# Optimization experiments

Measured on AMD Instinct MI355X. Metric: run time of the kernel, lower is better.

Reference implementation:

```python
import jax, jax.numpy as jnp
import numpy as np

B, C, H, W = 32, 192, 56, 56
DILATIONS = (1, 3, 5)
EPS = 1e-5


def setup_inputs() -> dict:
    key = jax.random.key(0)
    ks = jax.random.split(key, 4)
    x = jax.random.normal(ks[0], (B, C, H, W), dtype=jnp.float32)
    # learned params (per original torch init where it matters for math)
    bias = jnp.zeros((1, C, 1, 1), dtype=jnp.float32)            # LearnableBias
    conv_w = jax.random.normal(ks[1], (3, C, 1, 3, 3), dtype=jnp.float32) * 0.1  # depthwise kernels (OIHW, I=1)
    conv_b = jax.random.normal(ks[2], (3, C), dtype=jnp.float32) * 0.01
    move1 = jnp.zeros((3, C), dtype=jnp.float32)
    alpha = jnp.full((3, C), 0.25, dtype=jnp.float32)            # PReLU default init
    move2 = jnp.zeros((3, C), dtype=jnp.float32)
    ln_gamma = jnp.ones((C,), dtype=jnp.float32)
    ln_beta = jnp.zeros((C,), dtype=jnp.float32)
    return {"x": x, "bias": bias, "conv_w": conv_w, "conv_b": conv_b,
            "move1": move1, "alpha": alpha, "move2": move2,
            "ln_gamma": ln_gamma, "ln_beta": ln_beta}


def _per_ch(v):
    # (C,) -> (1,C,1,1) broadcastable over NCHW
    return v[None, :, None, None]


def reference(x, bias, conv_w, conv_b, move1, alpha, move2, ln_gamma, ln_beta):
    c = x.shape[1]
    xb = x + bias  # LearnableBias
    out = jnp.zeros_like(x)
    for i, d in enumerate(DILATIONS):
        # depthwise 3x3 dilated conv, 'same' padding => pad = d for k=3
        y = jax.lax.conv_general_dilated(
            xb, conv_w[i],
            window_strides=(1, 1),
            padding=((d, d), (d, d)),
            rhs_dilation=(d, d),
            feature_group_count=c,
            dimension_numbers=("NCHW", "OIHW", "NCHW"),
        ) + _per_ch(conv_b[i])
        # RPReLU: shift, per-channel PReLU, shift
        y = y - _per_ch(move1[i])
        y = jnp.where(y >= 0, y, _per_ch(alpha[i]) * y)
        y = y + _per_ch(move2[i])
        out = out + y
    # LayerNorm over channel dim (torch applies it on NHWC last axis == channels)
    mean = out.mean(axis=1, keepdims=True)
    var = out.var(axis=1, keepdims=True)  # biased, matches torch LayerNorm
    out = (out - mean) * jax.lax.rsqrt(var + EPS)
    out = out * _per_ch(ln_gamma) + _per_ch(ln_beta)
    return out
```

## Files before the change

kernel.cpp:

```cpp
#include <hip/hip_runtime.h>

#define C 192
#define H 56
#define W 56
#define HW (H * W)
#define CHW (C * HW)
#define NB 32
#define PPS 36
#define EPSLN 1e-5f

#define CTL_SHL1 0x101
#define CTL_SHL2 0x102
#define CTL_SHR1 0x111
#define CTL_SHR2 0x112

template<int CTRL>
__device__ __forceinline__ float dppf(float v) {
    return __int_as_float(__builtin_amdgcn_update_dpp(
        0, __float_as_int(v), CTRL, 0xf, 0xf, true));
}

struct __attribute__((aligned(16))) f4 { float x, y, z, w; };

__device__ __forceinline__ f4 f4z() { return {0.f, 0.f, 0.f, 0.f}; }
__device__ __forceinline__ f4 f4b(float s) { return {s, s, s, s}; }
__device__ __forceinline__ f4 fma4(f4 a, float s, f4 c) {
    return { fmaf(a.x, s, c.x), fmaf(a.y, s, c.y),
             fmaf(a.z, s, c.z), fmaf(a.w, s, c.w) };
}
__device__ __forceinline__ f4 shp1(f4 v){ return { v.y, v.z, v.w, dppf<CTL_SHL1>(v.x) }; }
__device__ __forceinline__ f4 shm1(f4 v){ return { dppf<CTL_SHR1>(v.w), v.x, v.y, v.z }; }
__device__ __forceinline__ f4 shp3(f4 v){ return { v.w, dppf<CTL_SHL1>(v.x),
                                                   dppf<CTL_SHL1>(v.y), dppf<CTL_SHL1>(v.z) }; }
__device__ __forceinline__ f4 shm3(f4 v){ return { dppf<CTL_SHR1>(v.y), dppf<CTL_SHR1>(v.z),
                                                   dppf<CTL_SHR1>(v.w), v.x }; }
__device__ __forceinline__ f4 shp5(f4 v){ return { dppf<CTL_SHL1>(v.y), dppf<CTL_SHL1>(v.z),
                                                   dppf<CTL_SHL1>(v.w), dppf<CTL_SHL2>(v.x) }; }
__device__ __forceinline__ f4 shm5(f4 v){ return { dppf<CTL_SHR2>(v.w), dppf<CTL_SHR1>(v.x),
                                                   dppf<CTL_SHR1>(v.y), dppf<CTL_SHR1>(v.z) }; }

__device__ __forceinline__ f4 prelu_acc(f4 acc, f4 y, float a) {
    acc.x += fmaxf(y.x, 0.f) + a * fminf(y.x, 0.f);
    acc.y += fmaxf(y.y, 0.f) + a * fminf(y.y, 0.f);
    acc.z += fmaxf(y.z, 0.f) + a * fminf(y.z, 0.f);
    acc.w += fmaxf(y.w, 0.f) + a * fminf(y.w, 0.f);
    return acc;
}

__global__ void prep_kernel(const float* __restrict__ bias,
                            const float* __restrict__ conv_w,
                            const float* __restrict__ conv_b,
                            const float* __restrict__ move1,
                            const float* __restrict__ alpha,
                            const float* __restrict__ move2,
                            const float* __restrict__ ln_g,
                            const float* __restrict__ ln_b,
                            float* __restrict__ pp, float* __restrict__ gb) {
    const int c = threadIdx.x;
    if (c >= C) return;
    float* pc = pp + c * PPS;
    #pragma unroll
    for (int i = 0; i < 3; ++i)
        #pragma unroll
        for (int k = 0; k < 9; ++k)
            pc[i * 9 + k] = conv_w[(size_t)(i * C + c) * 9 + k];
    #pragma unroll
    for (int i = 0; i < 3; ++i) {
        pc[27 + i] = conv_b[i * C + c] - move1[i * C + c];
        pc[30 + i] = alpha[i * C + c];
    }
    pc[33] = bias[c];
    pc[34] = move2[0 * C + c] + move2[1 * C + c] + move2[2 * C + c];
    pc[35] = 0.f;
    gb[2 * c]     = ln_g[c];
    gb[2 * c + 1] = ln_b[c];
}

__global__ __launch_bounds__(256, 3) void msgdc_kernel(
    const float* __restrict__ x, const float* __restrict__ pp,
    const float* __restrict__ gb, float* __restrict__ out)
{
    __shared__ float tile[C * W];
    __shared__ float sred[4][16][8];

    const int t = threadIdx.x;
    const int lane = t & 63;
    const int wv = __builtin_amdgcn_readfirstlane(t >> 6);
    const int l = lane & 15;
    const bool act = (l < 14);
    const float act_f = act ? 1.f : 0.f;
    const int lw = act ? 4 * l : 52;

    const int blk = blockIdx.x;
    const int gid = (blk & 7) * 224 + (blk >> 3);
    const int b = gid / H;
    const int h = gid - b * H;

    const bool vr[7] = { h >= 5, h >= 3, h >= 1, true,
                         h <= H - 2, h <= H - 4, h <= H - 6 };
    const int  ro[7] = { -5 * W, -3 * W, -1 * W, 0, 1 * W, 3 * W, 5 * W };
    float vm[7];
    #pragma unroll
    for (int k = 0; k < 7; ++k) vm[k] = vr[k] ? 1.f : 0.f;

    const int cbase = wv * 48 + (lane >> 4);
    const float* xc = x + (size_t)b * CHW + (size_t)cbase * HW + h * W + lw;

    f4 cur[7], nxt[7];
    #pragma unroll
    for (int k = 0; k < 7; ++k)
        nxt[k] = vr[k] ? *(const f4*)(xc + ro[k]) : f4z();

    f4 s4 = f4z(), q4 = f4z();

    #pragma unroll 2
    for (int j = 0; j < 12; ++j) {
        const int c = cbase + 4 * j;
        #pragma unroll
        for (int k = 0; k < 7; ++k) cur[k] = nxt[k];

        const float* pc = pp + c * PPS;
        float wf[36];
        #pragma unroll
        for (int k = 0; k < 9; ++k)
            *(f4*)(wf + 4 * k) = *(const f4*)(pc + 4 * k);

        if (j < 11) {
            const float* xn = xc + (size_t)(4 * (j + 1)) * HW;
            #pragma unroll
            for (int k = 0; k < 7; ++k)
                nxt[k] = vr[k] ? *(const f4*)(xn + ro[k]) : f4z();
        }

        const float bs = wf[33];
        f4 r[7];
        #pragma unroll
        for (int k = 0; k < 7; ++k) {
            const float bk = bs * vm[k] * act_f;
            r[k].x = fmaf(cur[k].x, act_f, bk);
            r[k].y = fmaf(cur[k].y, act_f, bk);
            r[k].z = fmaf(cur[k].z, act_f, bk);
            r[k].w = fmaf(cur[k].w, act_f, bk);
        }

        f4 acc = f4b(wf[34]);
        {
            f4 y = f4b(wf[27]);
            y = fma4(shm1(r[2]), wf[0], y);
            y = fma4(r[2],       wf[1], y);
            y = fma4(shp1(r[2]), wf[2], y);
            y = fma4(shm1(r[3]), wf[3], y);
            y = fma4(r[3],       wf[4], y);
            y = fma4(shp1(r[3]), wf[5], y);
            y = fma4(shm1(r[4]), wf[6], y);
            y = fma4(r[4],       wf[7], y);
            y = fma4(shp1(r[4]), wf[8], y);
            acc = prelu_acc(acc, y, wf[30]);
        }
        {
            f4 y = f4b(wf[28]);
            y = fma4(shm3(r[1]), wf[9],  y);
            y = fma4(r[1],       wf[10], y);
            y = fma4(shp3(r[1]), wf[11], y);
            y = fma4(shm3(r[3]), wf[12], y);
            y = fma4(r[3],       wf[13], y);
            y = fma4(shp3(r[3]), wf[14], y);
            y = fma4(shm3(r[5]), wf[15], y);
            y = fma4(r[5],       wf[16], y);
            y = fma4(shp3(r[5]), wf[17], y);
            acc = prelu_acc(acc, y, wf[31]);
        }
        {
            f4 y = f4b(wf[29]);
            y = fma4(shm5(r[0]), wf[18], y);
            y = fma4(r[0],       wf[19], y);
            y = fma4(shp5(r[0]), wf[20], y);
            y = fma4(shm5(r[3]), wf[21], y);
            y = fma4(r[3],       wf[22], y);
            y = fma4(shp5(r[3]), wf[23], y);
            y = fma4(shm5(r[6]), wf[24], y);
            y = fma4(r[6],       wf[25], y);
            y = fma4(shp5(r[6]), wf[26], y);
            acc = prelu_acc(acc, y, wf[32]);
        }

        s4.x += acc.x; s4.y += acc.y; s4.z += acc.z; s4.w += acc.w;
        q4.x = fmaf(acc.x, acc.x, q4.x); q4.y = fmaf(acc.y, acc.y, q4.y);
        q4.z = fmaf(acc.z, acc.z, q4.z); q4.w = fmaf(acc.w, acc.w, q4.w);

        if (act) *(f4*)(tile + c * W + lw) = acc;
    }

    #pragma unroll
    for (int m = 16; m <= 32; m <<= 1) {
        s4.x += __shfl_xor(s4.x, m, 64); s4.y += __shfl_xor(s4.y, m, 64);
        s4.z += __shfl_xor(s4.z, m, 64); s4.w += __shfl_xor(s4.w, m, 64);
        q4.x += __shfl_xor(q4.x, m, 64); q4.y += __shfl_xor(q4.y, m, 64);
        q4.z += __shfl_xor(q4.z, m, 64); q4.w += __shfl_xor(q4.w, m, 64);
    }
    if (lane < 14) {
        *(f4*)&sred[wv][lane][0] = s4;
        *(f4*)&sred[wv][lane][4] = q4;
    }
    __syncthreads();

    f4 S = f4z(), Q = f4z();
    #pragma unroll
    for (int w2 = 0; w2 < 4; ++w2) {
        const f4 a = *(const f4*)&sred[w2][l][0];
        const f4 bq = *(const f4*)&sred[w2][l][4];
        S.x += a.x; S.y += a.y; S.z += a.z; S.w += a.w;
        Q.x += bq.x; Q.y += bq.y; Q.z += bq.z; Q.w += bq.w;
    }
    const float inv = 1.f / (float)C;
    f4 mean = { S.x * inv, S.y * inv, S.z * inv, S.w * inv };
    f4 rstd = { rsqrtf(Q.x * inv - mean.x * mean.x + EPSLN),
                rsqrtf(Q.y * inv - mean.y * mean.y + EPSLN),
                rsqrtf(Q.z * inv - mean.z * mean.z + EPSLN),
                rsqrtf(Q.w * inv - mean.w * mean.w + EPSLN) };

    float* ob = out + (size_t)b * CHW + (size_t)cbase * HW + h * W + lw;
    #pragma unroll 2
    for (int j = 0; j < 12; ++j) {
        const int c = cbase + 4 * j;
        const float ga = gb[2 * c], be = gb[2 * c + 1];
        if (act) {
            const f4 v = *(const f4*)(tile + c * W + lw);
            f4 o;
            o.x = fmaf((v.x - mean.x) * rstd.x, ga, be);
            o.y = fmaf((v.y - mean.y) * rstd.y, ga, be);
            o.z = fmaf((v.z - mean.z) * rstd.z, ga, be);
            o.w = fmaf((v.w - mean.w) * rstd.w, ga, be);
            *(f4*)(ob + (size_t)(4 * j) * HW) = o;
        }
    }
}

extern "C" void kernel_launch(void* const* d_in, const int* in_sizes, int n_in,
                              void* d_out, int out_size, void* d_ws, size_t ws_size,
                              hipStream_t stream) {
    const float* x       = (const float*)d_in[0];
    const float* bias    = (const float*)d_in[1];
    const float* conv_w  = (const float*)d_in[2];
    const float* conv_b  = (const float*)d_in[3];
    const float* move1   = (const float*)d_in[4];
    const float* alpha   = (const float*)d_in[5];
    const float* move2   = (const float*)d_in[6];
    const float* ln_g    = (const float*)d_in[7];
    const float* ln_b    = (const float*)d_in[8];
    float* out = (float*)d_out;

    float* pp = (float*)d_ws;
    float* gbp = pp + C * PPS;

    prep_kernel<<<1, 256, 0, stream>>>(bias, conv_w, conv_b, move1, alpha,
                                       move2, ln_g, ln_b, pp, gbp);
    msgdc_kernel<<<NB * H, 256, 0, stream>>>(x, pp, gbp, out);
}
```

Before: 202.8 us.

## Store LayerNorm staging tile as bf16 and drop register prefetch for occupancy

The per-row intermediate tile in shared memory is stored as bf16 instead of fp32, which halves its LDS footprint. The register double-buffer that prefetched the next channel's seven input rows is removed, and the loop is no longer unrolled. Together these cut LDS and VGPR use so launch bounds can ask for 4 blocks per CU instead of 3, trading software prefetch for more wavefronts to hide memory latency. Rounding the pre-normalization values to bf16 adds precision error to the output.

```diff
diff --git a/kernel.cpp b/kernel.cpp
--- a/kernel.cpp
+++ b/kernel.cpp
@@ -21,6 +21,14 @@
 }
 
 struct __attribute__((aligned(16))) f4 { float x, y, z, w; };
+struct __attribute__((aligned(8))) us4 { unsigned short x, y, z, w; };
+
+__device__ __forceinline__ unsigned short f2bf(float v) {
+    return (unsigned short)((__float_as_uint(v) + 0x8000u) >> 16);
+}
+__device__ __forceinline__ float bf2f(unsigned short u) {
+    return __uint_as_float(((unsigned int)u) << 16);
+}
 
 __device__ __forceinline__ f4 f4z() { return {0.f, 0.f, 0.f, 0.f}; }
 __device__ __forceinline__ f4 f4b(float s) { return {s, s, s, s}; }
@@ -76,11 +84,11 @@
     gb[2 * c + 1] = ln_b[c];
 }
 
-__global__ __launch_bounds__(256, 3) void msgdc_kernel(
+__global__ __launch_bounds__(256, 4) void msgdc_kernel(
     const float* __restrict__ x, const float* __restrict__ pp,
     const float* __restrict__ gb, float* __restrict__ out)
 {
-    __shared__ float tile[C * W];
+    __shared__ unsigned short tile[C * W];
     __shared__ float sred[4][16][8];
 
     const int t = threadIdx.x;
@@ -104,20 +112,19 @@
     for (int k = 0; k < 7; ++k) vm[k] = vr[k] ? 1.f : 0.f;
 
     const int cbase = wv * 48 + (lane >> 4);
-    const float* xc = x + (size_t)b * CHW + (size_t)cbase * HW + h * W + lw;
-
-    f4 cur[7], nxt[7];
-    #pragma unroll
-    for (int k = 0; k < 7; ++k)
-        nxt[k] = vr[k] ? *(const f4*)(xc + ro[k]) : f4z();
+    const float* xc0 = x + (size_t)b * CHW + (size_t)cbase * HW + h * W + lw;
 
     f4 s4 = f4z(), q4 = f4z();
 
-    #pragma unroll 2
+    #pragma unroll 1
     for (int j = 0; j < 12; ++j) {
         const int c = cbase + 4 * j;
-        #pragma unroll
-        for (int k = 0; k < 7; ++k) cur[k] = nxt[k];
+
+        const float* xc = xc0 + (size_t)(4 * j) * HW;
+        f4 r[7];
+        #pragma unroll
+        for (int k = 0; k < 7; ++k)
+            r[k] = vr[k] ? *(const f4*)(xc + ro[k]) : f4z();
 
         const float* pc = pp + c * PPS;
         float wf[36];
@@ -125,22 +132,14 @@
         for (int k = 0; k < 9; ++k)
             *(f4*)(wf + 4 * k) = *(const f4*)(pc + 4 * k);
 
-        if (j < 11) {
-            const float* xn = xc + (size_t)(4 * (j + 1)) * HW;
-            #pragma unroll
-            for (int k = 0; k < 7; ++k)
-                nxt[k] = vr[k] ? *(const f4*)(xn + ro[k]) : f4z();
-        }
-
         const float bs = wf[33];
-        f4 r[7];
         #pragma unroll
         for (int k = 0; k < 7; ++k) {
             const float bk = bs * vm[k] * act_f;
-            r[k].x = fmaf(cur[k].x, act_f, bk);
-            r[k].y = fmaf(cur[k].y, act_f, bk);
-            r[k].z = fmaf(cur[k].z, act_f, bk);
-            r[k].w = fmaf(cur[k].w, act_f, bk);
+            r[k].x = fmaf(r[k].x, act_f, bk);
+            r[k].y = fmaf(r[k].y, act_f, bk);
+            r[k].z = fmaf(r[k].z, act_f, bk);
+            r[k].w = fmaf(r[k].w, act_f, bk);
         }
 
         f4 acc = f4b(wf[34]);
@@ -188,7 +187,10 @@
         q4.x = fmaf(acc.x, acc.x, q4.x); q4.y = fmaf(acc.y, acc.y, q4.y);
         q4.z = fmaf(acc.z, acc.z, q4.z); q4.w = fmaf(acc.w, acc.w, q4.w);
 
-        if (act) *(f4*)(tile + c * W + lw) = acc;
+        if (act) {
+            us4 p = { f2bf(acc.x), f2bf(acc.y), f2bf(acc.z), f2bf(acc.w) };
+            *(us4*)(tile + c * W + lw) = p;
+        }
     }
 
     #pragma unroll
@@ -225,12 +227,12 @@
         const int c = cbase + 4 * j;
         const float ga = gb[2 * c], be = gb[2 * c + 1];
         if (act) {
-            const f4 v = *(const f4*)(tile + c * W + lw);
+            const us4 p = *(const us4*)(tile + c * W + lw);
             f4 o;
-            o.x = fmaf((v.x - mean.x) * rstd.x, ga, be);
-            o.y = fmaf((v.y - mean.y) * rstd.y, ga, be);
-            o.z = fmaf((v.z - mean.z) * rstd.z, ga, be);
-            o.w = fmaf((v.w - mean.w) * rstd.w, ga, be);
+            o.x = fmaf((bf2f(p.x) - mean.x) * rstd.x, ga, be);
+            o.y = fmaf((bf2f(p.y) - mean.y) * rstd.y, ga, be);
+            o.z = fmaf((bf2f(p.z) - mean.z) * rstd.z, ga, be);
+            o.w = fmaf((bf2f(p.w) - mean.w) * rstd.w, ga, be);
             *(f4*)(ob + (size_t)(4 * j) * HW) = o;
         }
     }
```

After: 202.9 us. About the same (+0.0%).
